# Kernel optimization log

Measured on AMD Instinct MI355X. Metric: run time of the kernel, lower is better.

The kernel has to match this reference:

```python
import jax, jax.numpy as jnp
import numpy as np
from jax import lax

V, H, B, S, N, E = 32000, 128, 8, 512, 50000, 600000


def lstm(x, W_ih, W_hh, b):
    # x: [B,T,D]; W_ih: [4H,D]; W_hh: [4H,H]; b: [4H] (b_ih+b_hh combined)
    Bsz = x.shape[0]
    Hd = W_hh.shape[1]
    xg = jnp.einsum('btd,gd->btg', x, W_ih) + b  # precompute input gates [B,T,4H]
    h0 = jnp.zeros((Bsz, Hd), x.dtype)
    c0 = jnp.zeros((Bsz, Hd), x.dtype)

    def step(carry, g_t):
        h, c = carry
        g = g_t + h @ W_hh.T
        i, f, gg, o = jnp.split(g, 4, axis=-1)
        i = jax.nn.sigmoid(i)
        f = jax.nn.sigmoid(f)
        gg = jnp.tanh(gg)
        o = jax.nn.sigmoid(o)
        c = f * c + i * gg
        h = o * jnp.tanh(c)
        return (h, c), h

    _, hs = lax.scan(step, (h0, c0), jnp.swapaxes(xg, 0, 1))
    return jnp.swapaxes(hs, 0, 1)  # [B,T,H]


def gcn_conv(x, W, b, src, dst, n_nodes):
    # PyG GCNConv: add self-loops, symmetric normalization, out = A_hat (x W) + b
    h = x @ W.T  # [N,H]
    deg = jax.ops.segment_sum(jnp.ones(src.shape[0], x.dtype), dst, num_segments=n_nodes) + 1.0
    dinv = lax.rsqrt(deg)
    norm = dinv[src] * dinv[dst]  # [E]
    agg = jax.ops.segment_sum(h[src] * norm[:, None], dst, num_segments=n_nodes)
    agg = agg + h * (dinv * dinv)[:, None]  # self-loop contribution
    return agg + b


def setup_inputs() -> dict:
    key = jax.random.key(0)
    ks = jax.random.split(key, 20)
    s = 0.02
    return {
        'json_input': jax.random.randint(ks[0], (B, S), 0, V, dtype=jnp.int32),
        'node_ids': jax.random.randint(ks[1], (N,), 0, V, dtype=jnp.int32),
        'edge_index': jax.random.randint(ks[2], (2, E), 0, N, dtype=jnp.int32),
        'embedding': jax.random.normal(ks[3], (V, H), jnp.float32) * s,
        'W_ih_enc': jax.random.normal(ks[4], (4 * H, H), jnp.float32) * s,
        'W_hh_enc': jax.random.normal(ks[5], (4 * H, H), jnp.float32) * s,
        'b_enc': jnp.zeros((4 * H,), jnp.float32),
        'W1': jax.random.normal(ks[6], (H, H), jnp.float32) * s,
        'b1': jnp.zeros((H,), jnp.float32),
        'W2': jax.random.normal(ks[7], (H, H), jnp.float32) * s,
        'b2': jnp.zeros((H,), jnp.float32),
        'Wf': jax.random.normal(ks[8], (H, 2 * H), jnp.float32) * s,
        'bf': jnp.zeros((H,), jnp.float32),
        'W_ih_dec': jax.random.normal(ks[9], (4 * H, H), jnp.float32) * s,
        'W_hh_dec': jax.random.normal(ks[10], (4 * H, H), jnp.float32) * s,
        'b_dec': jnp.zeros((4 * H,), jnp.float32),
        'Wo': jax.random.normal(ks[11], (V, H), jnp.float32) * s,
        'bo': jnp.zeros((V,), jnp.float32),
    }


def reference(json_input, node_ids, edge_index, embedding, W_ih_enc, W_hh_enc, b_enc,
              W1, b1, W2, b2, Wf, bf, W_ih_dec, W_hh_dec, b_dec, Wo, bo):
    src, dst = edge_index[0], edge_index[1]
    # sequence branch
    json_emb = embedding[json_input]                      # [B,S,H]
    json_encoded = lstm(json_emb, W_ih_enc, W_hh_enc, b_enc)  # [B,S,H]
    # graph branch
    node_x = embedding[node_ids]                          # [N,H]
    x = gcn_conv(node_x, W1, b1, src, dst, node_ids.shape[0])
    x = gcn_conv(x, W2, b2, src, dst, node_ids.shape[0])
    # fusion
    graph_summary = jnp.broadcast_to(x.mean(axis=0, keepdims=True), (json_encoded.shape[0], x.shape[1]))
    combined = jnp.concatenate([json_encoded.mean(axis=1), graph_summary], axis=1)  # [B,2H]
    fused = combined @ Wf.T + bf                          # [B,H]
    fused_seq = jnp.broadcast_to(fused[:, None, :], (fused.shape[0], json_input.shape[1], fused.shape[1]))
    # decode
    decoded = lstm(fused_seq, W_ih_dec, W_hh_dec, b_dec)  # [B,S,H]
    return decoded @ Wo.T + bo                            # [B,S,V]
```

## Files before the change

### kernel.cpp

```cpp
#include <hip/hip_runtime.h>
#include <hip/hip_bf16.h>
#include <stdint.h>

#define VV 32000
#define HH 128
#define BB 8
#define SS 512
#define NNODE 50000
#define NEDGE 600000
#define NWORK 120
#define NOWN 125

typedef __attribute__((ext_vector_type(8))) short s16x8;
typedef __attribute__((ext_vector_type(4))) float f32x4;

__device__ __forceinline__ void workers_barrier(int* bar, int tid) {
  __syncthreads();
  if (tid == 0) {
    int g = __hip_atomic_load(&bar[32], __ATOMIC_ACQUIRE, __HIP_MEMORY_SCOPE_AGENT);
    int old = __hip_atomic_fetch_add(&bar[0], 1, __ATOMIC_ACQ_REL, __HIP_MEMORY_SCOPE_AGENT);
    if (old == NWORK-1) {
      __hip_atomic_store(&bar[0], 0, __ATOMIC_RELAXED, __HIP_MEMORY_SCOPE_AGENT);
      __hip_atomic_store(&bar[32], g+1, __ATOMIC_RELEASE, __HIP_MEMORY_SCOPE_AGENT);
    } else {
      while (__hip_atomic_load(&bar[32], __ATOMIC_ACQUIRE, __HIP_MEMORY_SCOPE_AGENT) == g)
        __builtin_amdgcn_s_sleep(32);
    }
  }
  __syncthreads();
}

__device__ __forceinline__ int ntload_i(const int* p) {
  return __builtin_nontemporal_load(p);
}
__device__ __forceinline__ float ntload_f(const float* p) {
  return __builtin_nontemporal_load(p);
}

__global__ __launch_bounds__(256) void xg_enc_kernel(
    const int* __restrict__ jin, const float* __restrict__ emb,
    const float* __restrict__ Wih, const float* __restrict__ bvec,
    float* __restrict__ xg)
{
  __shared__ __align__(16) float arow[8][128];
  const int tid = threadIdx.x, blk = blockIdx.x;
  {
    int r = tid >> 5, c = (tid & 31) << 2;
    int tok = jin[blk*8 + r];
    *(float4*)&arow[r][c] = *(const float4*)&emb[(size_t)tok*HH + c];
  }
  __syncthreads();
  const int g0 = tid * 2;
  const float* w0 = Wih + (size_t)g0*HH;
  const float* w1 = w0 + HH;
  float acc0[8], acc1[8];
  #pragma unroll
  for (int r=0;r<8;r++){ acc0[r]=0.f; acc1[r]=0.f; }
  for (int k=0;k<HH;k+=4) {
    float4 wa = *(const float4*)&w0[k];
    float4 wb = *(const float4*)&w1[k];
    #pragma unroll
    for (int r=0;r<8;r++) {
      float4 av = *(const float4*)&arow[r][k];
      acc0[r] += av.x*wa.x + av.y*wa.y + av.z*wa.z + av.w*wa.w;
      acc1[r] += av.x*wb.x + av.y*wb.y + av.z*wb.z + av.w*wb.w;
    }
  }
  float bb0 = bvec[g0], bb1 = bvec[g0+1];
  #pragma unroll
  for (int r=0;r<8;r++) {
    size_t row = (size_t)blk*8 + r;
    xg[row*512 + g0]     = acc0[r] + bb0;
    xg[row*512 + g0 + 1] = acc1[r] + bb1;
  }
}

__global__ __launch_bounds__(512) void front_kernel(
    const float* __restrict__ xg, const float* __restrict__ WhhE, float* __restrict__ hmean,
    const float* __restrict__ Wo, __hip_bfloat16* __restrict__ Bhi, __hip_bfloat16* __restrict__ Blo,
    const int* __restrict__ esrc, const int* __restrict__ edst, const int* __restrict__ nids,
    const float* __restrict__ emb,
    float* __restrict__ deg, float* __restrict__ dinv, float* __restrict__ s1,
    float* __restrict__ s2, float* __restrict__ cc, float* __restrict__ ee,
    float* __restrict__ csum, float* __restrict__ gvec,
    const float* __restrict__ W1, const float* __restrict__ b1,
    const float* __restrict__ W2, const float* __restrict__ b2, float* __restrict__ mvec,
    int* bar)
{
  __shared__ __align__(16) char shraw[131072];
  const int bid = blockIdx.x, tid = threadIdx.x;

  if (bid < 8) {
    float* h_s   = (float*)shraw;
    float* act_s = ((float*)shraw) + 128;
    const int b = bid;

    const f32x4* Wrow = (const f32x4*)(WhhE + (size_t)tid*HH);
    f32x4 w[32];
    #pragma unroll
    for (int k=0;k<32;k++) w[k] = Wrow[k];
    #pragma unroll
    for (int k=0;k<32;k++) asm volatile("" : "+v"(w[k]));

    const float* xgrow = xg + (size_t)b*SS*512;
    float xv = xgrow[tid];
    if (tid < 128) h_s[tid] = 0.f;
    float cstate = 0.f, hsum = 0.f;
    __syncthreads();

    for (int t=0;t<SS;t++) {
      int tn = (t < SS-1) ? (t+1) : t;
      float nxv = xgrow[(size_t)tn*512 + tid];
      float a0=0.f,a1=0.f,a2=0.f,a3=0.f;
      #pragma unroll
      for (int k=0;k<32;k++) {
        f32x4 hv = *(const f32x4*)&h_s[k*4];
        a0 += w[k].x*hv.x; a1 += w[k].y*hv.y;
        a2 += w[k].z*hv.z; a3 += w[k].w*hv.w;
      }
      float s = (a0+a1)+(a2+a3) + xv;
      int gid = tid >> 7;
      float act = (gid==2) ? tanhf(s) : 1.0f/(1.0f+expf(-s));
      act_s[tid] = act;
      __syncthreads();
      if (tid < 128) {
        float i_ = act_s[tid], f_ = act_s[128+tid], g_ = act_s[256+tid], o_ = act_s[384+tid];
        cstate = f_*cstate + i_*g_;
        float hh = o_*tanhf(cstate);
        h_s[tid] = hh;
        hsum += hh;
      }
      xv = nxv;
      __syncthreads();
    }
    if (tid < 128) hmean[b*HH + tid] = hsum * (1.0f/512.0f);
  } else {
    const int wbid = bid - 8;
    float* red = (float*)shraw;

    for (int i = wbid*512 + tid; i < VV*HH/4; i += NWORK*512) {
      f32x4 v = __builtin_nontemporal_load((const f32x4*)&Wo[i*4]);
      float vv[4] = {v.x, v.y, v.z, v.w};
      #pragma unroll
      for (int k=0;k<4;k++) {
        __hip_bfloat16 h = __float2bfloat16(vv[k]);
        float rem = vv[k] - __bfloat162float(h);
        __hip_bfloat16 l = __float2bfloat16(rem);
        __builtin_nontemporal_store(*(unsigned short*)&h, (unsigned short*)&Bhi[i*4+k]);
        __builtin_nontemporal_store(*(unsigned short*)&l, (unsigned short*)&Blo[i*4+k]);
      }
    }
    workers_barrier(bar, tid);
    for (int i = wbid*512 + tid; i < NEDGE; i += NWORK*512)
      atomicAdd(&deg[ntload_i(&edst[i])], 1.0f);
    workers_barrier(bar, tid);
    for (int n = wbid*512 + tid; n < NNODE; n += NWORK*512)
      dinv[n] = 1.0f / sqrtf(ntload_f(&deg[n]) + 1.0f);
    workers_barrier(bar, tid);
    for (int i = wbid*512 + tid; i < NEDGE; i += NWORK*512)
      atomicAdd(&s1[ntload_i(&esrc[i])], dinv[ntload_i(&edst[i])]);
    workers_barrier(bar, tid);
    {
      float lsum = 0.f;
      for (int n = wbid*512 + tid; n < NNODE; n += NWORK*512) {
        float d = ntload_f(&dinv[n]); float v = d*ntload_f(&s1[n]) + d*d;
        cc[n] = v; lsum += v;
      }
      red[tid] = lsum; __syncthreads();
      for (int sfl=256; sfl>0; sfl>>=1) { if (tid < sfl) red[tid] += red[tid+sfl]; __syncthreads(); }
      if (tid==0) atomicAdd(csum, red[0]);
    }
    workers_barrier(bar, tid);
    for (int i = wbid*512 + tid; i < NEDGE; i += NWORK*512) {
      int d = ntload_i(&edst[i]);
      atomicAdd(&s2[ntload_i(&esrc[i])], cc[d]*dinv[d]);
    }
    workers_barrier(bar, tid);
    for (int n = wbid*512 + tid; n < NNODE; n += NWORK*512) {
      float d = ntload_f(&dinv[n]);
      ee[n] = d*ntload_f(&s2[n]) + ntload_f(&cc[n])*d*d;
    }
    workers_barrier(bar, tid);
    {
      int j = tid & 127, sub = tid >> 7;
      float acc = 0.f;
      for (int n = wbid*4 + sub; n < NNODE; n += NWORK*4)
        acc += ntload_f(&ee[n]) * ntload_f(&emb[(size_t)ntload_i(&nids[n])*HH + j]);
      red[tid] = acc; __syncthreads();
      if (tid < 128) atomicAdd(&gvec[j], red[tid] + red[tid+128] + red[tid+256] + red[tid+384]);
    }
    workers_barrier(bar, tid);
    if (wbid == 0) {
      float* gs = (float*)shraw;
      float* v1 = gs + 128;
      if (tid < 128) gs[tid] = gvec[tid];
      __syncthreads();
      if (tid < 128) {
        float a = 0.f;
        for (int k=0;k<128;k++) a += gs[k]*W1[tid*128+k];
        v1[tid] = a + csum[0]*b1[tid];
      }
      __syncthreads();
      if (tid < 128) {
        float a2 = 0.f;
        for (int k=0;k<128;k++) a2 += v1[k]*W2[tid*128+k];
        mvec[tid] = a2 * (1.0f/(float)NNODE) + b2[tid];
      }
    }
  }
}

__global__ __launch_bounds__(512) void dec_gemm_kernel(
    const float* __restrict__ hmean, const float* __restrict__ mvec,
    const float* __restrict__ Wf, const float* __restrict__ bfv,
    const float* __restrict__ Wihd, const float* __restrict__ bd,
    const float* __restrict__ Whh,
    __hip_bfloat16* __restrict__ ahi, __hip_bfloat16* __restrict__ alo,
    const __hip_bfloat16* __restrict__ Bhi, const __hip_bfloat16* __restrict__ Blo,
    const float* __restrict__ bo, float* __restrict__ out, int* __restrict__ prog)
{
  __shared__ __align__(16) char shraw[131072];
  const int bid = blockIdx.x, tid = threadIdx.x;

  if (bid < 8) {
    float* h_s   = (float*)shraw;
    float* act_s = ((float*)shraw) + 128;
    float* fus   = (float*)(shraw + 4096);
    const int b = bid;

    const f32x4* Wrow = (const f32x4*)(Whh + (size_t)tid*HH);
    f32x4 w[32];
    #pragma unroll
    for (int k=0;k<32;k++) w[k] = Wrow[k];
    #pragma unroll
    for (int k=0;k<32;k++) asm volatile("" : "+v"(w[k]));

    float* comb = act_s;
    if (tid < 128) comb[tid] = hmean[b*128 + tid];
    else if (tid < 256) comb[tid] = mvec[tid - 128];
    __syncthreads();
    if (tid < 128) {
      float a = 0.f;
      for (int k=0;k<256;k++) a += comb[k]*Wf[tid*256+k];
      fus[tid] = a + bfv[tid];
    }
    __syncthreads();
    float xv;
    {
      float a = 0.f;
      for (int k=0;k<128;k++) a += fus[k]*Wihd[tid*128+k];
      xv = a + bd[tid];
    }
    __syncthreads();
    if (tid < 128) h_s[tid] = 0.f;
    float cstate = 0.f;
    __syncthreads();

    for (int t=0;t<SS;t++) {
      float a0=0.f,a1=0.f,a2=0.f,a3=0.f;
      #pragma unroll
      for (int k=0;k<32;k++) {
        f32x4 hv = *(const f32x4*)&h_s[k*4];
        a0 += w[k].x*hv.x; a1 += w[k].y*hv.y;
        a2 += w[k].z*hv.z; a3 += w[k].w*hv.w;
      }
      float s = (a0+a1)+(a2+a3) + xv;
      int gid = tid >> 7;
      float act = (gid==2) ? tanhf(s) : 1.0f/(1.0f+expf(-s));
      act_s[tid] = act;
      __syncthreads();
      if (tid < 128) {
        float i_ = act_s[tid], f_ = act_s[128+tid], g_ = act_s[256+tid], o_ = act_s[384+tid];
        cstate = f_*cstate + i_*g_;
        float hh = o_*tanhf(cstate);
        h_s[tid] = hh;
        size_t row = (size_t)b*SS + t;
        __hip_bfloat16 hi = __float2bfloat16(hh);
        float rem = hh - __bfloat162float(hi);
        __hip_bfloat16 lo = __float2bfloat16(rem);
        __builtin_nontemporal_store(*(unsigned short*)&hi, (unsigned short*)&ahi[row*HH + tid]);
        __builtin_nontemporal_store(*(unsigned short*)&lo, (unsigned short*)&alo[row*HH + tid]);
      }
      __syncthreads();
      if ((t & 63) == 63) {
        __threadfence();
        __syncthreads();
        if (tid == 0)
          __hip_atomic_store(&prog[b*32], (t >> 6) + 1,
                             __ATOMIC_RELEASE, __HIP_MEMORY_SCOPE_AGENT);
      }
    }
  } else {
    short* smem = (short*)shraw;
    const int nblk = bid - 8;

    const short* bsrc[2] = {
      (const short*)Bhi + (size_t)nblk*256*HH,
      (const short*)Blo + (size_t)nblk*256*HH };
    #pragma unroll
    for (int p=0;p<2;p++) {
      #pragma unroll
      for (int it=0; it<8; it++) {
        int off  = it*8192 + tid*16;
        int row  = off >> 8;
        int soff = off ^ ((row & 15) << 4);
        __builtin_amdgcn_global_load_lds(
          (const __attribute__((address_space(1))) void*)((const char*)bsrc[p] + soff),
          (__attribute__((address_space(3))) void*)((char*)smem + p*65536 + off),
          16, 0, 0);
      }
    }
    __syncthreads();

    const int lane = tid & 63;
    const int wid  = tid >> 6;
    const int wm = wid >> 2, wn = wid & 3;
    const int l15 = lane & 15, l4 = lane >> 4;
    const short* Ah = (const short*)ahi;
    const short* Al = (const short*)alo;

    for (int c = 0; c < 8; ++c) {
      for (int b = 0; b < 8; ++b) {
        if (tid == 0) {
          while (__hip_atomic_load(&prog[b*32], __ATOMIC_ACQUIRE,
                                   __HIP_MEMORY_SCOPE_AGENT) <= c)
            __builtin_amdgcn_s_sleep(64);
        }
        __syncthreads();

        const int mbase = b*512 + c*64 + wm*32;
        f32x4 acc[2][4] = {};
        #pragma unroll
        for (int s=0;s<4;s++) {
          s16x8 bh[4], bl[4], ah[2], al[2];
          #pragma unroll
          for (int qn=0;qn<4;qn++) {
            int rb   = wn*64 + qn*16 + l15;
            int offb = (rb*256 + s*64 + l4*16) ^ ((rb & 15) << 4);
            bh[qn] = *(const s16x8*)((const char*)smem + offb);
            bl[qn] = *(const s16x8*)((const char*)smem + 65536 + offb);
          }
          #pragma unroll
          for (int qm=0;qm<2;qm++) {
            int arow = mbase + qm*16 + l15;
            size_t aoff = (size_t)arow*HH + s*32 + l4*8;
            ah[qm] = *(const s16x8*)(Ah + aoff);
            al[qm] = *(const s16x8*)(Al + aoff);
          }
          #pragma unroll
          for (int qm=0;qm<2;qm++) {
            #pragma unroll
            for (int qn=0;qn<4;qn++) {
              acc[qm][qn] = __builtin_amdgcn_mfma_f32_16x16x32_bf16(bh[qn], ah[qm], acc[qm][qn], 0,0,0);
              acc[qm][qn] = __builtin_amdgcn_mfma_f32_16x16x32_bf16(bl[qn], ah[qm], acc[qm][qn], 0,0,0);
              acc[qm][qn] = __builtin_amdgcn_mfma_f32_16x16x32_bf16(bh[qn], al[qm], acc[qm][qn], 0,0,0);
            }
          }
        }
        if (c == 7) {
          #pragma unroll
          for (int qm=0;qm<2;qm++) {
            int row = mbase + qm*16 + l15;
            #pragma unroll
            for (int qn=0;qn<4;qn++) {
              int colb = nblk*256 + wn*64 + qn*16 + l4*4;
              f32x4 bv = *(const f32x4*)&bo[colb];
              f32x4 oo = acc[qm][qn] + bv;
              *(f32x4*)&out[(size_t)row*VV + colb] = oo;
            }
          }
        } else {
          #pragma unroll
          for (int qm=0;qm<2;qm++) {
            int row = mbase + qm*16 + l15;
            #pragma unroll
            for (int qn=0;qn<4;qn++) {
              int colb = nblk*256 + wn*64 + qn*16 + l4*4;
              f32x4 bv = *(const f32x4*)&bo[colb];
              f32x4 oo = acc[qm][qn] + bv;
              __builtin_nontemporal_store(oo, (f32x4*)&out[(size_t)row*VV + colb]);
            }
          }
        }
      }
    }
  }
}

extern "C" void kernel_launch(void* const* d_in, const int* in_sizes, int n_in,
                              void* d_out, int out_size, void* d_ws, size_t ws_size,
                              hipStream_t stream)
{
  (void)in_sizes; (void)n_in; (void)out_size; (void)ws_size;
  const int*   jin   = (const int*)d_in[0];
  const int*   nids  = (const int*)d_in[1];
  const int*   esrc  = (const int*)d_in[2];
  const int*   edst  = esrc + NEDGE;
  const float* emb   = (const float*)d_in[3];
  const float* WihE  = (const float*)d_in[4];
  const float* WhhE  = (const float*)d_in[5];
  const float* bE    = (const float*)d_in[6];
  const float* W1    = (const float*)d_in[7];
  const float* b1    = (const float*)d_in[8];
  const float* W2    = (const float*)d_in[9];
  const float* b2    = (const float*)d_in[10];
  const float* Wf    = (const float*)d_in[11];
  const float* bfv   = (const float*)d_in[12];
  const float* WihD  = (const float*)d_in[13];
  const float* WhhD  = (const float*)d_in[14];
  const float* bD    = (const float*)d_in[15];
  const float* Wo    = (const float*)d_in[16];
  const float* bo    = (const float*)d_in[17];
  float* out = (float*)d_out;

  char* ws = (char*)d_ws;
  size_t off = 0;
  auto alloc = [&](size_t bytes) { size_t o = off; off = (off + bytes + 255) & ~(size_t)255; return o; };

  int*   prog = (int*)(ws + alloc(BB*32*4));
  int*   bar  = (int*)(ws + alloc(64*4));
  float* deg  = (float*)(ws + alloc(NNODE*4));
  float* s1   = (float*)(ws + alloc(NNODE*4));
  float* s2   = (float*)(ws + alloc(NNODE*4));
  float* gvec = (float*)(ws + alloc(128*4));
  float* csum = (float*)(ws + alloc(4));
  size_t zero_bytes = off;
  float* dinv = (float*)(ws + alloc(NNODE*4));
  float* cc   = (float*)(ws + alloc(NNODE*4));
  float* ee   = (float*)(ws + alloc(NNODE*4));
  float* mvec = (float*)(ws + alloc(128*4));
  float* hmean= (float*)(ws + alloc(BB*HH*4));
  float* xgenc= (float*)(ws + alloc((size_t)BB*SS*512*4));
  __hip_bfloat16* Ahi = (__hip_bfloat16*)(ws + alloc((size_t)BB*SS*HH*2));
  __hip_bfloat16* Alo = (__hip_bfloat16*)(ws + alloc((size_t)BB*SS*HH*2));
  __hip_bfloat16* Bhi = (__hip_bfloat16*)(ws + alloc((size_t)VV*HH*2));
  __hip_bfloat16* Blo = (__hip_bfloat16*)(ws + alloc((size_t)VV*HH*2));

  hipMemsetAsync(ws, 0, zero_bytes, stream);

  xg_enc_kernel<<<dim3((BB*SS)/8), dim3(256), 0, stream>>>(jin, emb, WihE, bE, xgenc);

  front_kernel<<<dim3(8 + NWORK), dim3(512), 0, stream>>>(
      xgenc, WhhE, hmean, Wo, Bhi, Blo,
      esrc, edst, nids, emb, deg, dinv, s1, s2, cc, ee, csum, gvec,
      W1, b1, W2, b2, mvec, bar);

  dec_gemm_kernel<<<dim3(8 + NOWN), dim3(512), 0, stream>>>(
      hmean, mvec, Wf, bfv, WihD, bD, WhhD,
      Ahi, Alo, Bhi, Blo, bo, out, prog);
}
```

Measured before the change: 1.065 ms.

## Merge front and decoder/GEMM kernels into one persistent mega kernel

Fuses the encoder-LSTM/graph kernel and the decoder-LSTM/output-GEMM kernel into a single launch of 8+120+125 blocks. The LSTM blocks keep the encoder mean in shared memory and go straight into the decoder once a global flag signals that the graph worker blocks have finished mvec and the bf16 weight split. GEMM blocks spin on the same flag before loading the split weights. This removes one kernel launch and its boundary and lets the GEMM blocks be resident early, at the cost of needing all 253 blocks co-resident for the spin-waits to be safe, and of the decoder having to wait on a flag.

```diff
diff --git a/kernel.cpp b/kernel.cpp
--- a/kernel.cpp
+++ b/kernel.cpp
@@ -75,9 +75,13 @@
   }
 }
 
-__global__ __launch_bounds__(512) void front_kernel(
-    const float* __restrict__ xg, const float* __restrict__ WhhE, float* __restrict__ hmean,
-    const float* __restrict__ Wo, __hip_bfloat16* __restrict__ Bhi, __hip_bfloat16* __restrict__ Blo,
+__global__ __launch_bounds__(512) void mega_kernel(
+    const float* __restrict__ xg,
+    const float* __restrict__ WhhE, const float* __restrict__ WhhD,
+    const float* __restrict__ Wf, const float* __restrict__ bfv,
+    const float* __restrict__ Wihd, const float* __restrict__ bd,
+    const float* __restrict__ Wo,
+    __hip_bfloat16* __restrict__ Bhi, __hip_bfloat16* __restrict__ Blo,
     const int* __restrict__ esrc, const int* __restrict__ edst, const int* __restrict__ nids,
     const float* __restrict__ emb,
     float* __restrict__ deg, float* __restrict__ dinv, float* __restrict__ s1,
@@ -85,56 +89,132 @@
     float* __restrict__ csum, float* __restrict__ gvec,
     const float* __restrict__ W1, const float* __restrict__ b1,
     const float* __restrict__ W2, const float* __restrict__ b2, float* __restrict__ mvec,
-    int* bar)
+    __hip_bfloat16* __restrict__ ahi, __hip_bfloat16* __restrict__ alo,
+    const float* __restrict__ bo, float* __restrict__ out,
+    int* __restrict__ prog, int* __restrict__ bar)
 {
   __shared__ __align__(16) char shraw[131072];
   const int bid = blockIdx.x, tid = threadIdx.x;
+  int* gflag = prog + BB*32;
 
   if (bid < 8) {
     float* h_s   = (float*)shraw;
     float* act_s = ((float*)shraw) + 128;
+    float* fus   = (float*)(shraw + 4096);
     const int b = bid;
 
-    const f32x4* Wrow = (const f32x4*)(WhhE + (size_t)tid*HH);
-    f32x4 w[32];
-    #pragma unroll
-    for (int k=0;k<32;k++) w[k] = Wrow[k];
-    #pragma unroll
-    for (int k=0;k<32;k++) asm volatile("" : "+v"(w[k]));
-
-    const float* xgrow = xg + (size_t)b*SS*512;
-    float xv = xgrow[tid];
-    if (tid < 128) h_s[tid] = 0.f;
-    float cstate = 0.f, hsum = 0.f;
-    __syncthreads();
-
-    for (int t=0;t<SS;t++) {
-      int tn = (t < SS-1) ? (t+1) : t;
-      float nxv = xgrow[(size_t)tn*512 + tid];
-      float a0=0.f,a1=0.f,a2=0.f,a3=0.f;
-      #pragma unroll
-      for (int k=0;k<32;k++) {
-        f32x4 hv = *(const f32x4*)&h_s[k*4];
-        a0 += w[k].x*hv.x; a1 += w[k].y*hv.y;
-        a2 += w[k].z*hv.z; a3 += w[k].w*hv.w;
-      }
-      float s = (a0+a1)+(a2+a3) + xv;
-      int gid = tid >> 7;
-      float act = (gid==2) ? tanhf(s) : 1.0f/(1.0f+expf(-s));
-      act_s[tid] = act;
+    {
+      const f32x4* Wrow = (const f32x4*)(WhhE + (size_t)tid*HH);
+      f32x4 w[32];
+      #pragma unroll
+      for (int k=0;k<32;k++) w[k] = Wrow[k];
+      #pragma unroll
+      for (int k=0;k<32;k++) asm volatile("" : "+v"(w[k]));
+
+      const float* xgrow = xg + (size_t)b*SS*512;
+      float xv = xgrow[tid];
+      if (tid < 128) h_s[tid] = 0.f;
+      float cstate = 0.f, hsum = 0.f;
       __syncthreads();
-      if (tid < 128) {
-        float i_ = act_s[tid], f_ = act_s[128+tid], g_ = act_s[256+tid], o_ = act_s[384+tid];
-        cstate = f_*cstate + i_*g_;
-        float hh = o_*tanhf(cstate);
-        h_s[tid] = hh;
-        hsum += hh;
-      }
-      xv = nxv;
+
+      for (int t=0;t<SS;t++) {
+        int tn = (t < SS-1) ? (t+1) : t;
+        float nxv = xgrow[(size_t)tn*512 + tid];
+        float a0=0.f,a1=0.f,a2=0.f,a3=0.f;
+        #pragma unroll
+        for (int k=0;k<32;k++) {
+          f32x4 hv = *(const f32x4*)&h_s[k*4];
+          a0 += w[k].x*hv.x; a1 += w[k].y*hv.y;
+          a2 += w[k].z*hv.z; a3 += w[k].w*hv.w;
+        }
+        float s = (a0+a1)+(a2+a3) + xv;
+        int gid = tid >> 7;
+        float act = (gid==2) ? tanhf(s) : 1.0f/(1.0f+expf(-s));
+        act_s[tid] = act;
+        __syncthreads();
+        if (tid < 128) {
+          float i_ = act_s[tid], f_ = act_s[128+tid], g_ = act_s[256+tid], o_ = act_s[384+tid];
+          cstate = f_*cstate + i_*g_;
+          float hh = o_*tanhf(cstate);
+          h_s[tid] = hh;
+          hsum += hh;
+        }
+        xv = nxv;
+        __syncthreads();
+      }
+      if (tid < 128) act_s[tid] = hsum * (1.0f/512.0f);
+    }
+
+    if (tid == 0) {
+      while (__hip_atomic_load(gflag, __ATOMIC_ACQUIRE, __HIP_MEMORY_SCOPE_AGENT) == 0)
+        __builtin_amdgcn_s_sleep(32);
+    }
+    __syncthreads();
+    float* comb = act_s;
+    if (tid >= 128 && tid < 256) comb[tid] = mvec[tid - 128];
+    __syncthreads();
+    if (tid < 128) {
+      float a = 0.f;
+      for (int k=0;k<256;k++) a += comb[k]*Wf[tid*256+k];
+      fus[tid] = a + bfv[tid];
+    }
+    __syncthreads();
+    float xv;
+    {
+      float a = 0.f;
+      for (int k=0;k<128;k++) a += fus[k]*Wihd[tid*128+k];
+      xv = a + bd[tid];
+    }
+    __syncthreads();
+
+    {
+      const f32x4* Wrow = (const f32x4*)(WhhD + (size_t)tid*HH);
+      f32x4 w[32];
+      #pragma unroll
+      for (int k=0;k<32;k++) w[k] = Wrow[k];
+      #pragma unroll
+      for (int k=0;k<32;k++) asm volatile("" : "+v"(w[k]));
+
+      if (tid < 128) h_s[tid] = 0.f;
+      float cstate = 0.f;
       __syncthreads();
-    }
-    if (tid < 128) hmean[b*HH + tid] = hsum * (1.0f/512.0f);
-  } else {
+
+      for (int t=0;t<SS;t++) {
+        float a0=0.f,a1=0.f,a2=0.f,a3=0.f;
+        #pragma unroll
+        for (int k=0;k<32;k++) {
+          f32x4 hv = *(const f32x4*)&h_s[k*4];
+          a0 += w[k].x*hv.x; a1 += w[k].y*hv.y;
+          a2 += w[k].z*hv.z; a3 += w[k].w*hv.w;
+        }
+        float s = (a0+a1)+(a2+a3) + xv;
+        int gid = tid >> 7;
+        float act = (gid==2) ? tanhf(s) : 1.0f/(1.0f+expf(-s));
+        act_s[tid] = act;
+        __syncthreads();
+        if (tid < 128) {
+          float i_ = act_s[tid], f_ = act_s[128+tid], g_ = act_s[256+tid], o_ = act_s[384+tid];
+          cstate = f_*cstate + i_*g_;
+          float hh = o_*tanhf(cstate);
+          h_s[tid] = hh;
+          size_t row = (size_t)b*SS + t;
+          __hip_bfloat16 hi = __float2bfloat16(hh);
+          float rem = hh - __bfloat162float(hi);
+          __hip_bfloat16 lo = __float2bfloat16(rem);
+          __builtin_nontemporal_store(*(unsigned short*)&hi, (unsigned short*)&ahi[row*HH + tid]);
+          __builtin_nontemporal_store(*(unsigned short*)&lo, (unsigned short*)&alo[row*HH + tid]);
+        }
+        __syncthreads();
+        if ((t & 63) == 63) {
+          __threadfence();
+          __syncthreads();
+          if (tid == 0)
+            __hip_atomic_store(&prog[b*32], (t >> 6) + 1,
+                               __ATOMIC_RELEASE, __HIP_MEMORY_SCOPE_AGENT);
+        }
+      }
+    }
+  } else if (bid < 8 + NWORK) {
     const int wbid = bid - 8;
     float* red = (float*)shraw;
 
@@ -150,6 +230,7 @@
         __builtin_nontemporal_store(*(unsigned short*)&l, (unsigned short*)&Blo[i*4+k]);
       }
     }
+    __threadfence();
     workers_barrier(bar, tid);
     for (int i = wbid*512 + tid; i < NEDGE; i += NWORK*512)
       atomicAdd(&deg[ntload_i(&edst[i])], 1.0f);
@@ -206,93 +287,20 @@
         for (int k=0;k<128;k++) a2 += v1[k]*W2[tid*128+k];
         mvec[tid] = a2 * (1.0f/(float)NNODE) + b2[tid];
       }
-    }
-  }
-}
-
-__global__ __launch_bounds__(512) void dec_gemm_kernel(
-    const float* __restrict__ hmean, const float* __restrict__ mvec,
-    const float* __restrict__ Wf, const float* __restrict__ bfv,
-    const float* __restrict__ Wihd, const float* __restrict__ bd,
-    const float* __restrict__ Whh,
-    __hip_bfloat16* __restrict__ ahi, __hip_bfloat16* __restrict__ alo,
-    const __hip_bfloat16* __restrict__ Bhi, const __hip_bfloat16* __restrict__ Blo,
-    const float* __restrict__ bo, float* __restrict__ out, int* __restrict__ prog)
-{
-  __shared__ __align__(16) char shraw[131072];
-  const int bid = blockIdx.x, tid = threadIdx.x;
-
-  if (bid < 8) {
-    float* h_s   = (float*)shraw;
-    float* act_s = ((float*)shraw) + 128;
-    float* fus   = (float*)(shraw + 4096);
-    const int b = bid;
-
-    const f32x4* Wrow = (const f32x4*)(Whh + (size_t)tid*HH);
-    f32x4 w[32];
-    #pragma unroll
-    for (int k=0;k<32;k++) w[k] = Wrow[k];
-    #pragma unroll
-    for (int k=0;k<32;k++) asm volatile("" : "+v"(w[k]));
-
-    float* comb = act_s;
-    if (tid < 128) comb[tid] = hmean[b*128 + tid];
-    else if (tid < 256) comb[tid] = mvec[tid - 128];
-    __syncthreads();
-    if (tid < 128) {
-      float a = 0.f;
-      for (int k=0;k<256;k++) a += comb[k]*Wf[tid*256+k];
-      fus[tid] = a + bfv[tid];
-    }
-    __syncthreads();
-    float xv;
-    {
-      float a = 0.f;
-      for (int k=0;k<128;k++) a += fus[k]*Wihd[tid*128+k];
-      xv = a + bd[tid];
-    }
-    __syncthreads();
-    if (tid < 128) h_s[tid] = 0.f;
-    float cstate = 0.f;
-    __syncthreads();
-
-    for (int t=0;t<SS;t++) {
-      float a0=0.f,a1=0.f,a2=0.f,a3=0.f;
-      #pragma unroll
-      for (int k=0;k<32;k++) {
-        f32x4 hv = *(const f32x4*)&h_s[k*4];
-        a0 += w[k].x*hv.x; a1 += w[k].y*hv.y;
-        a2 += w[k].z*hv.z; a3 += w[k].w*hv.w;
-      }
-      float s = (a0+a1)+(a2+a3) + xv;
-      int gid = tid >> 7;
-      float act = (gid==2) ? tanhf(s) : 1.0f/(1.0f+expf(-s));
-      act_s[tid] = act;
       __syncthreads();
-      if (tid < 128) {
-        float i_ = act_s[tid], f_ = act_s[128+tid], g_ = act_s[256+tid], o_ = act_s[384+tid];
-        cstate = f_*cstate + i_*g_;
-        float hh = o_*tanhf(cstate);
-        h_s[tid] = hh;
-        size_t row = (size_t)b*SS + t;
-        __hip_bfloat16 hi = __float2bfloat16(hh);
-        float rem = hh - __bfloat162float(hi);
-        __hip_bfloat16 lo = __float2bfloat16(rem);
-        __builtin_nontemporal_store(*(unsigned short*)&hi, (unsigned short*)&ahi[row*HH + tid]);
-        __builtin_nontemporal_store(*(unsigned short*)&lo, (unsigned short*)&alo[row*HH + tid]);
-      }
-      __syncthreads();
-      if ((t & 63) == 63) {
-        __threadfence();
-        __syncthreads();
-        if (tid == 0)
-          __hip_atomic_store(&prog[b*32], (t >> 6) + 1,
-                             __ATOMIC_RELEASE, __HIP_MEMORY_SCOPE_AGENT);
-      }
+      __threadfence();
+      if (tid == 0)
+        __hip_atomic_store(gflag, 1, __ATOMIC_RELEASE, __HIP_MEMORY_SCOPE_AGENT);
     }
   } else {
     short* smem = (short*)shraw;
-    const int nblk = bid - 8;
+    const int nblk = bid - 8 - NWORK;
+
+    if (tid == 0) {
+      while (__hip_atomic_load(gflag, __ATOMIC_ACQUIRE, __HIP_MEMORY_SCOPE_AGENT) == 0)
+        __builtin_amdgcn_s_sleep(64);
+    }
+    __syncthreads();
 
     const short* bsrc[2] = {
       (const short*)Bhi + (size_t)nblk*256*HH,
@@ -417,7 +425,7 @@
   size_t off = 0;
   auto alloc = [&](size_t bytes) { size_t o = off; off = (off + bytes + 255) & ~(size_t)255; return o; };
 
-  int*   prog = (int*)(ws + alloc(BB*32*4));
+  int*   prog = (int*)(ws + alloc((BB+1)*32*4));
   int*   bar  = (int*)(ws + alloc(64*4));
   float* deg  = (float*)(ws + alloc(NNODE*4));
   float* s1   = (float*)(ws + alloc(NNODE*4));
@@ -429,7 +437,6 @@
   float* cc   = (float*)(ws + alloc(NNODE*4));
   float* ee   = (float*)(ws + alloc(NNODE*4));
   float* mvec = (float*)(ws + alloc(128*4));
-  float* hmean= (float*)(ws + alloc(BB*HH*4));
   float* xgenc= (float*)(ws + alloc((size_t)BB*SS*512*4));
   __hip_bfloat16* Ahi = (__hip_bfloat16*)(ws + alloc((size_t)BB*SS*HH*2));
   __hip_bfloat16* Alo = (__hip_bfloat16*)(ws + alloc((size_t)BB*SS*HH*2));
@@ -440,12 +447,8 @@
 
   xg_enc_kernel<<<dim3((BB*SS)/8), dim3(256), 0, stream>>>(jin, emb, WihE, bE, xgenc);
 
-  front_kernel<<<dim3(8 + NWORK), dim3(512), 0, stream>>>(
-      xgenc, WhhE, hmean, Wo, Bhi, Blo,
+  mega_kernel<<<dim3(8 + NWORK + NOWN), dim3(512), 0, stream>>>(
+      xgenc, WhhE, WhhD, Wf, bfv, WihD, bD, Wo, Bhi, Blo,
       esrc, edst, nids, emb, deg, dinv, s1, s2, cc, ee, csum, gvec,
-      W1, b1, W2, b2, mvec, bar);
-
-  dec_gemm_kernel<<<dim3(8 + NOWN), dim3(512), 0, stream>>>(
-      hmean, mvec, Wf, bfv, WihD, bD, WhhD,
-      Ahi, Alo, Bhi, Blo, bo, out, prog);
-}
+      W1, b1, W2, b2, mvec, Ahi, Alo, bo, out, prog, bar);
+}
```

New measurement: 1.099 ms. 3.2% more time.
